# Optimization experiments

Hardware: AMD Instinct MI355X
Metric: run time of the kernel (lower is better)

Reference implementation:

```python
import jax, jax.numpy as jnp
import numpy as np

N = 50000
E = 800000
D = 128          # node_dim
ED = 64          # edge_dim
H = 4            # n_heads
HD = D // H      # head_dim
LN_EPS = 1e-5


def setup_inputs() -> dict:
    key = jax.random.key(0)
    ks = jax.random.split(key, 10)
    s = 0.05
    return {
        "x": jax.random.normal(ks[0], (N, D), dtype=jnp.float32),
        "edge_index": jax.random.randint(ks[1], (2, E), 0, N, dtype=jnp.int32),
        "edge_attr": jax.random.normal(ks[2], (E, ED), dtype=jnp.float32),
        # parameters (torch Linear transposed to [in, out])
        "align_w": jax.random.normal(ks[3], (2 * D + ED, H), dtype=jnp.float32) * s,
        "align_b": jnp.zeros((H,), dtype=jnp.float32),
        "value_w": jax.random.normal(ks[4], (D, D), dtype=jnp.float32) * s,
        "value_b": jnp.zeros((D,), dtype=jnp.float32),
        "proj_w": jax.random.normal(ks[5], (D, D), dtype=jnp.float32) * s,
        "proj_b": jnp.zeros((D,), dtype=jnp.float32),
        "ln_g": jnp.ones((D,), dtype=jnp.float32),
        "ln_b": jnp.zeros((D,), dtype=jnp.float32),
    }


def reference(x, edge_index, edge_attr, align_w, align_b, value_w, value_b,
              proj_w, proj_b, ln_g, ln_b):
    row, col = edge_index[0], edge_index[1]          # [E], [E]
    h_i = x[row]                                     # [E, D] gather (dst)
    h_j = x[col]                                     # [E, D] gather (src)
    cat_feat = jnp.concatenate([h_i, h_j, edge_attr], axis=-1)  # [E, 2D+ED]
    scores = cat_feat @ align_w + align_b            # [E, H]

    # numerically-stable segment softmax over incoming edges of each dst node
    max_per_node = jax.ops.segment_max(scores, row, num_segments=N)  # [N, H]
    scores_exp = jnp.exp(scores - max_per_node[row])                 # [E, H]
    sum_exp = jax.ops.segment_sum(scores_exp, row, num_segments=N)   # [N, H]
    alpha = scores_exp / (sum_exp[row] + 1e-8)                       # [E, H]

    V = (h_j @ value_w + value_b).reshape(E, H, HD)                  # [E, H, HD]
    weighted = (V * alpha[:, :, None]).reshape(E, D)                 # [E, D]
    context = jax.ops.segment_sum(weighted, row, num_segments=N)     # [N, D]

    y = x + context @ proj_w + proj_b                                # [N, D]
    mu = jnp.mean(y, axis=-1, keepdims=True)
    var = jnp.mean((y - mu) ** 2, axis=-1, keepdims=True)
    return (y - mu) / jnp.sqrt(var + LN_EPS) * ln_g + ln_b
```

## Files before the change

kernel.cpp:

```cpp
#include <hip/hip_runtime.h>
#include <hip/hip_bf16.h>
#include <math.h>

#define N_NODES 50000
#define N_EDGES 800000
#define DIM 128
#define EDIM 64
#define NH 4
#define DEG_CAP 64
#define BKT_BLOCKS 3125
#define PRE_BLOCKS 1563

__global__ __launch_bounds__(256) void k_prep(
    const int* __restrict__ ei, int* cnt, int2* __restrict__ ecolid,
    const float* __restrict__ x, const float* __restrict__ vw,
    const float* __restrict__ vb, const float* __restrict__ aw,
    unsigned int* __restrict__ Vxb, float* __restrict__ a_src) {
    __shared__ float xs[32][129];
    int t = threadIdx.x;
    if (blockIdx.x < BKT_BLOCKS) {
        int e = blockIdx.x * 256 + t;
        if (e < N_EDGES) {
            int row = ei[e], col = ei[N_EDGES + e];
            int pos = atomicAdd(&cnt[row], 1);
            if (pos < DEG_CAP) ecolid[(size_t)row * DEG_CAP + pos] = make_int2(col, e);
        }
        return;
    }
    int nb = (blockIdx.x - BKT_BLOCKS) * 32;
    #pragma unroll
    for (int i = 0; i < 4; ++i) {
        int idx = i * 256 + t;
        int m = idx >> 5, k4 = idx & 31;
        int n = nb + m;
        float4 v = make_float4(0.f, 0.f, 0.f, 0.f);
        if (n < N_NODES) v = *(const float4*)(x + (size_t)n * DIM + k4 * 4);
        xs[m][k4*4+0] = v.x; xs[m][k4*4+1] = v.y; xs[m][k4*4+2] = v.z; xs[m][k4*4+3] = v.w;
    }
    __syncthreads();
    int c = t & 31, mg = t >> 5;
    int d0 = c * 4, m0 = mg * 4;
    float acc[4][4];
    #pragma unroll
    for (int j = 0; j < 4; ++j) { acc[j][0]=0.f; acc[j][1]=0.f; acc[j][2]=0.f; acc[j][3]=0.f; }
    for (int k = 0; k < DIM; ++k) {
        float4 w = *(const float4*)(vw + (size_t)k * DIM + d0);
        #pragma unroll
        for (int j = 0; j < 4; ++j) {
            float xv = xs[m0 + j][k];
            acc[j][0] += xv * w.x; acc[j][1] += xv * w.y;
            acc[j][2] += xv * w.z; acc[j][3] += xv * w.w;
        }
    }
    float4 vb4 = *(const float4*)(vb + d0);
    #pragma unroll
    for (int j = 0; j < 4; ++j) {
        int n = nb + m0 + j;
        if (n < N_NODES) {
            __hip_bfloat162 p0 = __float22bfloat162_rn(
                make_float2(acc[j][0]+vb4.x, acc[j][1]+vb4.y));
            __hip_bfloat162 p1 = __float22bfloat162_rn(
                make_float2(acc[j][2]+vb4.z, acc[j][3]+vb4.w));
            uint2 u;
            u.x = *reinterpret_cast<unsigned int*>(&p0);
            u.y = *reinterpret_cast<unsigned int*>(&p1);
            *(uint2*)(Vxb + (size_t)n * 64 + c * 2) = u;
        }
    }
    if (t < 128) {
        int m = t >> 2, h = t & 3;
        float s = 0.f;
        for (int k = 0; k < DIM; ++k) s += xs[m][k] * aw[(size_t)(DIM + k) * NH + h];
        int n = nb + m;
        if (n < N_NODES) a_src[(size_t)n * NH + h] = s;
    }
}

__global__ __launch_bounds__(256) void k_mega(
    const int* __restrict__ cnt, const int2* __restrict__ ecolid,
    const float* __restrict__ ea, const float* __restrict__ aw,
    const float* __restrict__ a_src, const unsigned int* __restrict__ Vxb,
    float* __restrict__ context) {
    int t = threadIdx.x;
    int lane = t & 63, w = t >> 6;
    int n = blockIdx.x * 4 + w;
    if (n >= N_NODES) return;
    int l = lane & 15, grp = lane >> 4;
    int hd = l >> 2;
    int trl = (lane & 48) | ((l & 3) << 2) | (l >> 2);
    float wreg[16];
    #pragma unroll
    for (int j = 0; j < 4; ++j)
        #pragma unroll
        for (int h = 0; h < NH; ++h)
            wreg[j * 4 + h] = aw[1024 + (l * 4 + j) * 4 + h];
    int deg = cnt[n]; deg = deg < DEG_CAP ? deg : DEG_CAP;
    int2 ce = (lane < deg) ? ecolid[(size_t)n * DEG_CAP + lane] : make_int2(0, 0);
    int colv = ce.x, eidv = ce.y;
    float a0=0.f,a1=0.f,a2=0.f,a3=0.f,a4=0.f,a5=0.f,a6=0.f,a7=0.f,sw=0.f;
    int jm4 = (deg + 3) & ~3;
    #pragma unroll 4
    for (int j = grp; j < jm4; j += 4) {
        int col = __shfl(colv, j);
        int eid = __shfl(eidv, j);
        float4 v = *(const float4*)(ea + (size_t)eid * EDIM + l * 4);
        float p0 = v.x*wreg[0] + v.y*wreg[4] + v.z*wreg[8]  + v.w*wreg[12];
        float p1 = v.x*wreg[1] + v.y*wreg[5] + v.z*wreg[9]  + v.w*wreg[13];
        float p2 = v.x*wreg[2] + v.y*wreg[6] + v.z*wreg[10] + v.w*wreg[14];
        float p3 = v.x*wreg[3] + v.y*wreg[7] + v.z*wreg[11] + v.w*wreg[15];
        #pragma unroll
        for (int off = 1; off < 4; off <<= 1) {
            p0 += __shfl_xor(p0, off);
            p1 += __shfl_xor(p1, off);
            p2 += __shfl_xor(p2, off);
            p3 += __shfl_xor(p3, off);
        }
        int r = l & 3;
        float pr = (r == 0) ? p0 : (r == 1) ? p1 : (r == 2) ? p2 : p3;
        pr += __shfl_xor(pr, 4);
        pr += __shfl_xor(pr, 8);
        float ph = __shfl(pr, trl);
        float s = ph + a_src[(size_t)col * NH + hd];
        float wgt = (j < deg) ? __expf(s) : 0.f;
        uint4 u = *(const uint4*)(Vxb + (size_t)col * 64 + l * 4);
        float f0 = __uint_as_float(u.x << 16), f1 = __uint_as_float(u.x & 0xffff0000u);
        float f2 = __uint_as_float(u.y << 16), f3 = __uint_as_float(u.y & 0xffff0000u);
        float f4 = __uint_as_float(u.z << 16), f5 = __uint_as_float(u.z & 0xffff0000u);
        float f6 = __uint_as_float(u.w << 16), f7 = __uint_as_float(u.w & 0xffff0000u);
        a0 += f0*wgt; a1 += f1*wgt; a2 += f2*wgt; a3 += f3*wgt;
        a4 += f4*wgt; a5 += f5*wgt; a6 += f6*wgt; a7 += f7*wgt;
        sw += wgt;
    }
    #pragma unroll
    for (int off = 16; off < 64; off <<= 1) {
        a0 += __shfl_xor(a0, off); a1 += __shfl_xor(a1, off);
        a2 += __shfl_xor(a2, off); a3 += __shfl_xor(a3, off);
        a4 += __shfl_xor(a4, off); a5 += __shfl_xor(a5, off);
        a6 += __shfl_xor(a6, off); a7 += __shfl_xor(a7, off);
        sw += __shfl_xor(sw, off);
    }
    if (lane < 16) {
        float inv = 1.0f / (sw + 1e-8f);
        float* cp = context + (size_t)n * DIM + l * 8;
        *(float4*)(cp)     = make_float4(a0*inv, a1*inv, a2*inv, a3*inv);
        *(float4*)(cp + 4) = make_float4(a4*inv, a5*inv, a6*inv, a7*inv);
    }
}

__global__ __launch_bounds__(128) void k_proj_ln(
    const float* __restrict__ x, const float* __restrict__ context,
    const float* __restrict__ pw, const float* __restrict__ pb,
    const float* __restrict__ lg, const float* __restrict__ lb,
    float* __restrict__ out) {
    __shared__ float cs[32][129];
    int t = threadIdx.x;
    int nb = blockIdx.x * 32;
    #pragma unroll
    for (int i = 0; i < 8; ++i) {
        int idx = i * 128 + t;
        int m = idx >> 5, k4 = idx & 31;
        int n = nb + m;
        float4 v = make_float4(0.f, 0.f, 0.f, 0.f);
        if (n < N_NODES) v = *(const float4*)(context + (size_t)n * DIM + k4 * 4);
        cs[m][k4*4+0] = v.x; cs[m][k4*4+1] = v.y; cs[m][k4*4+2] = v.z; cs[m][k4*4+3] = v.w;
    }
    __syncthreads();
    int c = t & 31, mg = t >> 5;
    int d0 = c * 4, m0 = mg * 8;
    float acc[8][4];
    #pragma unroll
    for (int j = 0; j < 8; ++j) { acc[j][0]=0.f; acc[j][1]=0.f; acc[j][2]=0.f; acc[j][3]=0.f; }
    for (int k = 0; k < DIM; ++k) {
        float4 w = *(const float4*)(pw + (size_t)k * DIM + d0);
        #pragma unroll
        for (int j = 0; j < 8; ++j) {
            float cv = cs[m0 + j][k];
            acc[j][0] += cv * w.x; acc[j][1] += cv * w.y;
            acc[j][2] += cv * w.z; acc[j][3] += cv * w.w;
        }
    }
    float4 pb4 = *(const float4*)(pb + d0);
    float4 g4  = *(const float4*)(lg + d0);
    float4 b4  = *(const float4*)(lb + d0);
    #pragma unroll
    for (int j = 0; j < 8; ++j) {
        int n = nb + m0 + j;
        float4 xv = make_float4(0.f, 0.f, 0.f, 0.f);
        if (n < N_NODES) xv = *(const float4*)(x + (size_t)n * DIM + d0);
        float y0 = xv.x + acc[j][0] + pb4.x;
        float y1 = xv.y + acc[j][1] + pb4.y;
        float y2 = xv.z + acc[j][2] + pb4.z;
        float y3 = xv.w + acc[j][3] + pb4.w;
        float ps = y0 + y1 + y2 + y3;
        float pq = y0*y0 + y1*y1 + y2*y2 + y3*y3;
        #pragma unroll
        for (int off = 1; off < 32; off <<= 1) {
            ps += __shfl_xor(ps, off);
            pq += __shfl_xor(pq, off);
        }
        float mu = ps * (1.0f / DIM);
        float var = pq * (1.0f / DIM) - mu * mu;
        float rstd = rsqrtf(var + 1e-5f);
        if (n < N_NODES) {
            float4 o;
            o.x = (y0 - mu) * rstd * g4.x + b4.x;
            o.y = (y1 - mu) * rstd * g4.y + b4.y;
            o.z = (y2 - mu) * rstd * g4.z + b4.z;
            o.w = (y3 - mu) * rstd * g4.w + b4.w;
            *(float4*)(out + (size_t)n * DIM + d0) = o;
        }
    }
}

extern "C" void kernel_launch(void* const* d_in, const int* in_sizes, int n_in,
                              void* d_out, int out_size, void* d_ws, size_t ws_size,
                              hipStream_t stream) {
    const float* x       = (const float*)d_in[0];
    const int*   ei      = (const int*)  d_in[1];
    const float* ea      = (const float*)d_in[2];
    const float* align_w = (const float*)d_in[3];
    const float* value_w = (const float*)d_in[5];
    const float* value_b = (const float*)d_in[6];
    const float* proj_w  = (const float*)d_in[7];
    const float* proj_b  = (const float*)d_in[8];
    const float* ln_g    = (const float*)d_in[9];
    const float* ln_b    = (const float*)d_in[10];
    float* out = (float*)d_out;
    float* ws  = (float*)d_ws;

    unsigned int* Vxb = (unsigned int*)ws;
    float* a_src   = ws + 3200000;
    float* context = ws + 3400000;
    int2*  ecolid  = (int2*)(ws + 9800000);
    int*   cnt     = (int*)(ws + 16200000);

    hipMemsetAsync(cnt, 0, (size_t)N_NODES * sizeof(int), stream);
    k_prep<<<BKT_BLOCKS + PRE_BLOCKS, 256, 0, stream>>>(
        ei, cnt, ecolid, x, value_w, value_b, align_w, Vxb, a_src);
    k_mega<<<(N_NODES + 3) / 4, 256, 0, stream>>>(
        cnt, ecolid, ea, align_w, a_src, Vxb, context);
    k_proj_ln<<<(N_NODES + 31) / 32, 128, 0, stream>>>(
        x, context, proj_w, proj_b, ln_g, ln_b, out);
}
```

Measured before the change: 215.7 us.

## Precompute per-edge exp scores in prep kernel and factor exp of sum

After: 228.0 us. 1.06x slower.

```diff
diff --git a/kernel.cpp b/kernel.cpp
--- a/kernel.cpp
+++ b/kernel.cpp
@@ -8,6 +8,7 @@
 #define EDIM 64
 #define NH 4
 #define DEG_CAP 64
+#define ESC_BLOCKS 12500
 #define BKT_BLOCKS 3125
 #define PRE_BLOCKS 1563
 
@@ -15,11 +16,44 @@
     const int* __restrict__ ei, int* cnt, int2* __restrict__ ecolid,
     const float* __restrict__ x, const float* __restrict__ vw,
     const float* __restrict__ vb, const float* __restrict__ aw,
-    unsigned int* __restrict__ Vxb, float* __restrict__ a_src) {
+    const float* __restrict__ ea, float* __restrict__ sexp,
+    unsigned int* __restrict__ Vxb, float* __restrict__ aexp) {
     __shared__ float xs[32][129];
     int t = threadIdx.x;
-    if (blockIdx.x < BKT_BLOCKS) {
-        int e = blockIdx.x * 256 + t;
+    if (blockIdx.x < ESC_BLOCKS) {
+        int l = t & 15, g = t >> 4;
+        float wreg[16];
+        #pragma unroll
+        for (int j = 0; j < 4; ++j)
+            #pragma unroll
+            for (int h = 0; h < NH; ++h)
+                wreg[j * 4 + h] = aw[1024 + (l * 4 + j) * 4 + h];
+        int e0 = blockIdx.x * 16 + g;
+        #pragma unroll
+        for (int k = 0; k < 4; ++k) {
+            int e = e0 + k * (ESC_BLOCKS * 16);
+            float4 v = *(const float4*)(ea + (size_t)e * EDIM + l * 4);
+            float p0 = v.x*wreg[0] + v.y*wreg[4] + v.z*wreg[8]  + v.w*wreg[12];
+            float p1 = v.x*wreg[1] + v.y*wreg[5] + v.z*wreg[9]  + v.w*wreg[13];
+            float p2 = v.x*wreg[2] + v.y*wreg[6] + v.z*wreg[10] + v.w*wreg[14];
+            float p3 = v.x*wreg[3] + v.y*wreg[7] + v.z*wreg[11] + v.w*wreg[15];
+            #pragma unroll
+            for (int off = 1; off < 4; off <<= 1) {
+                p0 += __shfl_xor(p0, off);
+                p1 += __shfl_xor(p1, off);
+                p2 += __shfl_xor(p2, off);
+                p3 += __shfl_xor(p3, off);
+            }
+            int r = l & 3;
+            float pr = (r == 0) ? p0 : (r == 1) ? p1 : (r == 2) ? p2 : p3;
+            pr += __shfl_xor(pr, 4);
+            pr += __shfl_xor(pr, 8);
+            if (l < 4) sexp[(size_t)e * 4 + l] = __expf(pr);
+        }
+        return;
+    }
+    if (blockIdx.x < ESC_BLOCKS + BKT_BLOCKS) {
+        int e = (blockIdx.x - ESC_BLOCKS) * 256 + t;
         if (e < N_EDGES) {
             int row = ei[e], col = ei[N_EDGES + e];
             int pos = atomicAdd(&cnt[row], 1);
@@ -27,7 +61,7 @@
         }
         return;
     }
-    int nb = (blockIdx.x - BKT_BLOCKS) * 32;
+    int nb = (blockIdx.x - ESC_BLOCKS - BKT_BLOCKS) * 32;
     #pragma unroll
     for (int i = 0; i < 4; ++i) {
         int idx = i * 256 + t;
@@ -72,28 +106,20 @@
         float s = 0.f;
         for (int k = 0; k < DIM; ++k) s += xs[m][k] * aw[(size_t)(DIM + k) * NH + h];
         int n = nb + m;
-        if (n < N_NODES) a_src[(size_t)n * NH + h] = s;
+        if (n < N_NODES) aexp[(size_t)n * NH + h] = __expf(s);
     }
 }
 
 __global__ __launch_bounds__(256) void k_mega(
     const int* __restrict__ cnt, const int2* __restrict__ ecolid,
-    const float* __restrict__ ea, const float* __restrict__ aw,
-    const float* __restrict__ a_src, const unsigned int* __restrict__ Vxb,
-    float* __restrict__ context) {
+    const float* __restrict__ sexp, const float* __restrict__ aexp,
+    const unsigned int* __restrict__ Vxb, float* __restrict__ context) {
     int t = threadIdx.x;
     int lane = t & 63, w = t >> 6;
     int n = blockIdx.x * 4 + w;
     if (n >= N_NODES) return;
     int l = lane & 15, grp = lane >> 4;
     int hd = l >> 2;
-    int trl = (lane & 48) | ((l & 3) << 2) | (l >> 2);
-    float wreg[16];
-    #pragma unroll
-    for (int j = 0; j < 4; ++j)
-        #pragma unroll
-        for (int h = 0; h < NH; ++h)
-            wreg[j * 4 + h] = aw[1024 + (l * 4 + j) * 4 + h];
     int deg = cnt[n]; deg = deg < DEG_CAP ? deg : DEG_CAP;
     int2 ce = (lane < deg) ? ecolid[(size_t)n * DEG_CAP + lane] : make_int2(0, 0);
     int colv = ce.x, eidv = ce.y;
@@ -103,25 +129,9 @@
     for (int j = grp; j < jm4; j += 4) {
         int col = __shfl(colv, j);
         int eid = __shfl(eidv, j);
-        float4 v = *(const float4*)(ea + (size_t)eid * EDIM + l * 4);
-        float p0 = v.x*wreg[0] + v.y*wreg[4] + v.z*wreg[8]  + v.w*wreg[12];
-        float p1 = v.x*wreg[1] + v.y*wreg[5] + v.z*wreg[9]  + v.w*wreg[13];
-        float p2 = v.x*wreg[2] + v.y*wreg[6] + v.z*wreg[10] + v.w*wreg[14];
-        float p3 = v.x*wreg[3] + v.y*wreg[7] + v.z*wreg[11] + v.w*wreg[15];
-        #pragma unroll
-        for (int off = 1; off < 4; off <<= 1) {
-            p0 += __shfl_xor(p0, off);
-            p1 += __shfl_xor(p1, off);
-            p2 += __shfl_xor(p2, off);
-            p3 += __shfl_xor(p3, off);
-        }
-        int r = l & 3;
-        float pr = (r == 0) ? p0 : (r == 1) ? p1 : (r == 2) ? p2 : p3;
-        pr += __shfl_xor(pr, 4);
-        pr += __shfl_xor(pr, 8);
-        float ph = __shfl(pr, trl);
-        float s = ph + a_src[(size_t)col * NH + hd];
-        float wgt = (j < deg) ? __expf(s) : 0.f;
+        float wgt = 0.f;
+        if (j < deg)
+            wgt = sexp[(size_t)eid * 4 + hd] * aexp[(size_t)col * NH + hd];
         uint4 u = *(const uint4*)(Vxb + (size_t)col * 64 + l * 4);
         float f0 = __uint_as_float(u.x << 16), f1 = __uint_as_float(u.x & 0xffff0000u);
         float f2 = __uint_as_float(u.y << 16), f3 = __uint_as_float(u.y & 0xffff0000u);
@@ -229,16 +239,17 @@
     float* ws  = (float*)d_ws;
 
     unsigned int* Vxb = (unsigned int*)ws;
-    float* a_src   = ws + 3200000;
-    float* context = ws + 3400000;
-    int2*  ecolid  = (int2*)(ws + 9800000);
-    int*   cnt     = (int*)(ws + 16200000);
+    float* aexp    = ws + 3200000;
+    float* sexp    = ws + 3400000;
+    float* context = ws + 6600000;
+    int2*  ecolid  = (int2*)(ws + 13000000);
+    int*   cnt     = (int*)(ws + 19400000);
 
     hipMemsetAsync(cnt, 0, (size_t)N_NODES * sizeof(int), stream);
-    k_prep<<<BKT_BLOCKS + PRE_BLOCKS, 256, 0, stream>>>(
-        ei, cnt, ecolid, x, value_w, value_b, align_w, Vxb, a_src);
-    k_mega<<<(N_NODES + 3) / 4, 256, 0, stream>>>(
-        cnt, ecolid, ea, align_w, a_src, Vxb, context);
+    k_prep<<<ESC_BLOCKS + BKT_BLOCKS + PRE_BLOCKS, 256, 0, stream>>>(
+        ei, cnt, ecolid, x, value_w, value_b, align_w, ea, sexp, Vxb, aexp);
+    k_mega<<<N_NODES / 4, 256, 0, stream>>>(
+        cnt, ecolid, sexp, aexp, Vxb, context);
     k_proj_ln<<<(N_NODES + 31) / 32, 128, 0, stream>>>(
         x, context, proj_w, proj_b, ln_g, ln_b, out);
 }
```
